# Performance work log

Measured on AMD Instinct MI355X. Metric: run time of the kernel, lower is better.

## Reference

```python
import jax, jax.numpy as jnp
import numpy as np

NEG = -1e30  # finite stand-in for -inf (keeps gradients NaN-free)
BLANK = 0    # PyTorch nn.CTCLoss default blank index


def setup_inputs() -> dict:
    key = jax.random.key(0)
    k1, k2, k3 = jax.random.split(key, 3)
    T, B, C, S = 512, 1024, 63, 25
    # model emits log-probabilities (log_softmax output), as nn.CTCLoss expects
    log_probs = jax.nn.log_softmax(jax.random.normal(k1, (T, B, C), jnp.float32), axis=-1)
    targets = jax.random.randint(k2, (B, S), 1, C, dtype=jnp.int32)        # labels in [1, C)
    target_lengths = jax.random.randint(k3, (B,), 10, S + 1, dtype=jnp.int32)
    return {"log_probs": log_probs, "targets": targets, "target_lengths": target_lengths}


def _ctc_loss(log_probs, targets, target_lengths):
    # log_probs: [T, B, C]; targets: [B, S] padded; target_lengths: [B]
    T, B, C = log_probs.shape
    S = targets.shape[1]
    L = 2 * S + 1  # extended target: blank-interleaved

    ext = jnp.zeros((B, L), targets.dtype).at[:, 1::2].set(targets)  # [B, L]
    prev2 = jnp.concatenate([jnp.full((B, 2), -1, ext.dtype), ext[:, :-2]], axis=1)
    skip = (ext != BLANK) & (ext != prev2)  # allow alpha[s-2] transition

    # t = 0 init: only positions 0 (blank) and 1 (first label) reachable
    lp0 = log_probs[0]  # [B, C]
    alpha0 = jnp.full((B, L), NEG, log_probs.dtype)
    alpha0 = alpha0.at[:, 0].set(lp0[:, BLANK])
    alpha0 = alpha0.at[:, 1].set(jnp.take_along_axis(lp0, ext[:, 1:2], axis=1)[:, 0])

    def step(alpha, lp_t):  # alpha: [B, L], lp_t: [B, C]
        lp_ext = jnp.take_along_axis(lp_t, ext, axis=1)  # [B, L]
        a1 = alpha
        a2 = jnp.pad(alpha[:, :-1], ((0, 0), (1, 0)), constant_values=NEG)
        a3 = jnp.where(skip, jnp.pad(alpha[:, :-2], ((0, 0), (2, 0)), constant_values=NEG), NEG)
        m = jnp.maximum(jnp.maximum(a1, a2), a3)
        new = m + jnp.log(jnp.exp(a1 - m) + jnp.exp(a2 - m) + jnp.exp(a3 - m)) + lp_ext
        return new, None

    alpha_T, _ = jax.lax.scan(step, alpha0, log_probs[1:])

    # log-likelihood = logaddexp of the last two reachable positions (2*len, 2*len-1)
    idx = jnp.stack([2 * target_lengths - 1, 2 * target_lengths], axis=1)  # [B, 2]
    a_fin = jnp.take_along_axis(alpha_T, idx, axis=1)
    ll = jnp.logaddexp(a_fin[:, 0], a_fin[:, 1])
    nll = -ll
    nll = jnp.where(nll > 0.5e30, 0.0, nll)  # zero_infinity=True
    # PyTorch reduction='mean': divide each loss by its target length, then batch mean
    return jnp.mean(nll / jnp.maximum(target_lengths, 1).astype(nll.dtype))


def reference(log_probs, targets, target_lengths):
    return _ctc_loss(log_probs, targets, target_lengths)
```

## Files before the change

### kernel.cpp

```cpp
#include <hip/hip_runtime.h>


#define TT 512
#define BB 1024
#define CC 63
#define SS 25
#define D  32
#define NEGV (-1e30f)
#define LN2F 0.69314718055994531f

__device__ __forceinline__ float shr1f(float x, float fill) {
  return __int_as_float(__builtin_amdgcn_update_dpp(
      __float_as_int(fill), __float_as_int(x), 0x138, 0xF, 0xF, false));
}
__device__ __forceinline__ int shr1i(int x, int fill) {
  return __builtin_amdgcn_update_dpp(fill, x, 0x138, 0xF, 0xF, false);
}
__device__ __forceinline__ float shl1f(float x, float fill) {
  return __int_as_float(__builtin_amdgcn_update_dpp(
      __float_as_int(fill), __float_as_int(x), 0x130, 0xF, 0xF, false));
}
__device__ __forceinline__ int shl1i(int x, int fill) {
  return __builtin_amdgcn_update_dpp(fill, x, 0x130, 0xF, 0xF, false);
}
__device__ __forceinline__ int iclamp126(int d) {
  return d < -126 ? -126 : (d > 126 ? 126 : d);
}

__global__ __launch_bounds__(256) void ctc_fb_kernel(
    const float* __restrict__ logp,
    const int* __restrict__ targets,
    const int* __restrict__ tlen,
    float* __restrict__ loss) {
  const int lane = threadIdx.x & 63;
  const int wid = threadIdx.x >> 6;
  const int pairIdx = wid >> 1;
  const int bwd = wid & 1;
  const int b = (blockIdx.x << 1) + pairIdx;
  const int* tg = targets + b * SS;
  const int len = tlen[b];

  int e = 0;
  float skf = 0.0f;
  float skf2 = 0.0f;
  if (lane & 1) {
    const int i = lane >> 1;
    if (i < SS) {
      e = tg[i];
      skf = (i == 0 || e != tg[i - 1]) ? 1.0f : 0.0f;
      if (i + 1 < SS) skf2 = (tg[i + 1] != tg[i]) ? 1.0f : 0.0f;
    }
  }

  const unsigned SB = (unsigned)(BB * CC) * 4u;
  const char* base = (const char*)logp;
  const unsigned off0 = (unsigned)(b * CC + e) * 4u;
#define LDF(O) (*(const float*)(base + (O)))

  __shared__ float la_s[2][64];

  float A, F1, F2m;
  int M2 = 0;
  float pf[D];
  unsigned offp;

  if (!bwd) {
    A = (lane <= 1) ? __expf(LDF(off0)) : 0.0f;
    F1 = 1.0f; F2m = skf;
    offp = off0 + SB;
#pragma unroll
    for (int j = 0; j < D; ++j) { pf[j] = LDF(offp); offp += SB; }

#define RENF() {                                               \
    int e2 = (int)(__float_as_uint(A) >> 23) - 127;            \
    A = ldexpf(A, -e2);                                        \
    int m2n = M2 + e2;                                         \
    int m2a = shr1i(m2n, 0);                                   \
    M2 = (A == 0.0f) ? m2a : m2n;                              \
    int s1 = shr1i(M2, 0), s2 = shr1i(s1, 0);                  \
    F1 = ldexpf(1.0f, iclamp126(s1 - M2));                     \
    F2m = skf * ldexpf(1.0f, iclamp126(s2 - M2));              \
  }
#define STEPF(J, PFLAG) {                                      \
    const float P = __expf(pf[(J)]);                           \
    const float c1 = P * F1, c2 = P * F2m;                     \
    const float a2 = shr1f(A, 0.0f);                           \
    const float pa = P * A;                                    \
    const float a3 = shr1f(a2, 0.0f);                          \
    A = fmaf(c2, a3, fmaf(c1, a2, pa));                        \
    if (PFLAG) { pf[(J)] = LDF(offp); offp += SB; }            \
    if (((J) & 15) == 15) RENF()                               \
  }

    for (int blk = 0; blk < 6; ++blk) {
#pragma unroll
      for (int j = 0; j < D; ++j) STEPF(j, true)
    }
#pragma unroll
    for (int j = 0; j < D; ++j) STEPF(j, j < 31)
#pragma unroll
    for (int j = 0; j < 31; ++j) STEPF(j, false)

    la_s[pairIdx][lane] = fmaxf((float)M2 * LN2F + logf(A), NEGV);
  } else {
    A = (lane == 2 * len - 1 || lane == 2 * len) ? 1.0f : 0.0f;
    F1 = 1.0f; F2m = skf2;
    offp = 511u * SB + off0;
#pragma unroll
    for (int j = 0; j < D; ++j) { pf[j] = LDF(offp); offp -= SB; }

#define RENB() {                                               \
    int e2 = (int)(__float_as_uint(A) >> 23) - 127;            \
    A = ldexpf(A, -e2);                                        \
    int m2n = M2 + e2;                                         \
    int m2a = shl1i(m2n, 0);                                   \
    M2 = (A == 0.0f) ? m2a : m2n;                              \
    int s1 = shl1i(M2, 0), s2 = shl1i(s1, 0);                  \
    F1 = ldexpf(1.0f, iclamp126(s1 - M2));                     \
    F2m = skf2 * ldexpf(1.0f, iclamp126(s2 - M2));             \
  }
#define STEPB(J, PFLAG) {                                      \
    const float P = __expf(pf[(J)]);                           \
    const float P1 = shl1f(P, 0.0f);                           \
    const float P2 = shl1f(P1, 0.0f);                          \
    const float c1 = F1 * P1, c2 = F2m * P2;                   \
    const float a1 = shl1f(A, 0.0f);                           \
    const float pa = P * A;                                    \
    const float a2 = shl1f(a1, 0.0f);                          \
    A = fmaf(c2, a2, fmaf(c1, a1, pa));                        \
    if (PFLAG) { pf[(J)] = LDF(offp); offp -= SB; }            \
    if (((J) & 15) == 15) RENB()                               \
  }

    for (int blk = 0; blk < 7; ++blk) {
#pragma unroll
      for (int j = 0; j < D; ++j) STEPB(j, true)
    }
#pragma unroll
    for (int j = 0; j < D; ++j) STEPB(j, false)
  }

  __syncthreads();

  if (bwd) {
    const float lb = fmaxf((float)M2 * LN2F + logf(A), NEGV);
    float v = (lane <= 50) ? la_s[pairIdx][lane] + lb : -2e30f;
    float m = v;
#pragma unroll
    for (int o = 32; o; o >>= 1) m = fmaxf(m, __shfl_xor(m, o));
    float s = __expf(v - m);
#pragma unroll
    for (int o = 32; o; o >>= 1) s += __shfl_xor(s, o);
    if (lane == 0) {
      const float ll = m + logf(s);
      float nll = -ll;
      if (!(nll <= 0.5e30f)) nll = 0.0f;
      const int dl = len > 1 ? len : 1;
      loss[b] = nll / (float)dl;
    }
  }
}

__global__ __launch_bounds__(256) void ctc_reduce_kernel(
    const float* __restrict__ loss, float* __restrict__ out) {
  float s = 0.f;
  for (int i = threadIdx.x; i < BB; i += 256) s += loss[i];
#pragma unroll
  for (int off = 32; off; off >>= 1) s += __shfl_down(s, off);
  __shared__ float sm[4];
  if ((threadIdx.x & 63) == 0) sm[threadIdx.x >> 6] = s;
  __syncthreads();
  if (threadIdx.x == 0) out[0] = (sm[0] + sm[1] + sm[2] + sm[3]) / (float)BB;
}

extern "C" void kernel_launch(void* const* d_in, const int* in_sizes, int n_in,
                              void* d_out, int out_size, void* d_ws, size_t ws_size,
                              hipStream_t stream) {
  const float* logp  = (const float*)d_in[0];
  const int* targets = (const int*)d_in[1];
  const int* tlen    = (const int*)d_in[2];
  float* out  = (float*)d_out;
  float* loss = (float*)d_ws;
  hipLaunchKernelGGL(ctc_fb_kernel, dim3(BB / 2), dim3(256), 0, stream,
                     logp, targets, tlen, loss);
  hipLaunchKernelGGL(ctc_reduce_kernel, dim3(1), dim3(256), 0, stream, loss, out);
}
```

Baseline: 32.92 us.

## Interleave forward and backward CTC recursions within a single wavefront per batch

Each wavefront now handles one batch element and runs both the forward alpha and backward beta recursions interleaved, instead of splitting them across two wavefronts joined through shared memory and a block barrier. The two independent dependency chains are meant to hide each other's DPP and FMA latency, and the barrier and LDS exchange go away. Prefetch depth per direction drops to 24 registers to fit both buffers. The cost is half as many wavefronts in total, so there is less latency hiding across waves, and register pressure goes up.

Result: faster. 31.96 us (median of 2 runs) (-2.9%).

```diff
diff --git a/kernel.cpp b/kernel.cpp
--- a/kernel.cpp
+++ b/kernel.cpp
@@ -5,7 +5,7 @@
 #define BB 1024
 #define CC 63
 #define SS 25
-#define D  32
+#define DP 24
 #define NEGV (-1e30f)
 #define LN2F 0.69314718055994531f
 
@@ -34,9 +34,7 @@
     float* __restrict__ loss) {
   const int lane = threadIdx.x & 63;
   const int wid = threadIdx.x >> 6;
-  const int pairIdx = wid >> 1;
-  const int bwd = wid & 1;
-  const int b = (blockIdx.x << 1) + pairIdx;
+  const int b = (blockIdx.x << 2) + wid;
   const int* tg = targets + b * SS;
   const int len = tlen[b];
 
@@ -55,109 +53,103 @@
   const unsigned SB = (unsigned)(BB * CC) * 4u;
   const char* base = (const char*)logp;
   const unsigned off0 = (unsigned)(b * CC + e) * 4u;
-#define LDF(O) (*(const float*)(base + (O)))
+#define LDR(O) (*(const float*)(base + (O)))
 
-  __shared__ float la_s[2][64];
+  float Af = (lane <= 1) ? __expf(LDR(off0)) : 0.0f;
+  int M2f = 0;
+  float F1f = 1.0f, F2f = skf;
+  float Ab = (lane == 2 * len - 1 || lane == 2 * len) ? 1.0f : 0.0f;
+  int M2b = 0;
+  float F1b = 1.0f, F2b = skf2;
 
-  float A, F1, F2m;
-  int M2 = 0;
-  float pf[D];
-  unsigned offp;
-
-  if (!bwd) {
-    A = (lane <= 1) ? __expf(LDF(off0)) : 0.0f;
-    F1 = 1.0f; F2m = skf;
-    offp = off0 + SB;
+  float pfF[DP], pfB[DP];
+  unsigned offF = off0 + SB;
+  unsigned offB = off0 + 511u * SB;
 #pragma unroll
-    for (int j = 0; j < D; ++j) { pf[j] = LDF(offp); offp += SB; }
+  for (int j = 0; j < DP; ++j) {
+    pfF[j] = LDR(offF); offF += SB;
+    pfB[j] = LDR(offB); offB -= SB;
+  }
 
 #define RENF() {                                               \
-    int e2 = (int)(__float_as_uint(A) >> 23) - 127;            \
-    A = ldexpf(A, -e2);                                        \
-    int m2n = M2 + e2;                                         \
+    int e2 = (int)(__float_as_uint(Af) >> 23) - 127;           \
+    Af = ldexpf(Af, -e2);                                      \
+    int m2n = M2f + e2;                                        \
     int m2a = shr1i(m2n, 0);                                   \
-    M2 = (A == 0.0f) ? m2a : m2n;                              \
-    int s1 = shr1i(M2, 0), s2 = shr1i(s1, 0);                  \
-    F1 = ldexpf(1.0f, iclamp126(s1 - M2));                     \
-    F2m = skf * ldexpf(1.0f, iclamp126(s2 - M2));              \
+    M2f = (Af == 0.0f) ? m2a : m2n;                            \
+    int s1 = shr1i(M2f, 0), s2 = shr1i(s1, 0);                 \
+    F1f = ldexpf(1.0f, iclamp126(s1 - M2f));                   \
+    F2f = skf * ldexpf(1.0f, iclamp126(s2 - M2f));             \
+  }
+#define RENB() {                                               \
+    int e2 = (int)(__float_as_uint(Ab) >> 23) - 127;           \
+    Ab = ldexpf(Ab, -e2);                                      \
+    int m2n = M2b + e2;                                        \
+    int m2a = shl1i(m2n, 0);                                   \
+    M2b = (Ab == 0.0f) ? m2a : m2n;                            \
+    int s1 = shl1i(M2b, 0), s2 = shl1i(s1, 0);                 \
+    F1b = ldexpf(1.0f, iclamp126(s1 - M2b));                   \
+    F2b = skf2 * ldexpf(1.0f, iclamp126(s2 - M2b));            \
   }
 #define STEPF(J, PFLAG) {                                      \
-    const float P = __expf(pf[(J)]);                           \
-    const float c1 = P * F1, c2 = P * F2m;                     \
-    const float a2 = shr1f(A, 0.0f);                           \
-    const float pa = P * A;                                    \
-    const float a3 = shr1f(a2, 0.0f);                          \
-    A = fmaf(c2, a3, fmaf(c1, a2, pa));                        \
-    if (PFLAG) { pf[(J)] = LDF(offp); offp += SB; }            \
-    if (((J) & 15) == 15) RENF()                               \
+    const float P = __expf(pfF[(J)]);                          \
+    const float c1 = P * F1f, c2 = P * F2f;                    \
+    const float x1 = shr1f(Af, 0.0f);                          \
+    const float pa = P * Af;                                   \
+    const float x2 = shr1f(x1, 0.0f);                          \
+    Af = fmaf(c2, x2, fmaf(c1, x1, pa));                       \
+    if (PFLAG) { pfF[(J)] = LDR(offF); offF += SB; }           \
+  }
+#define STEPB(J, PFLAG) {                                      \
+    const float P = __expf(pfB[(J)]);                          \
+    const float P1 = shl1f(P, 0.0f);                           \
+    const float P2 = shl1f(P1, 0.0f);                          \
+    const float c1 = F1b * P1, c2 = F2b * P2;                  \
+    const float y1 = shl1f(Ab, 0.0f);                          \
+    const float pb = P * Ab;                                   \
+    const float y2 = shl1f(y1, 0.0f);                          \
+    Ab = fmaf(c2, y2, fmaf(c1, y1, pb));                       \
+    if (PFLAG) { pfB[(J)] = LDR(offB); offB -= SB; }           \
   }
 
-    for (int blk = 0; blk < 6; ++blk) {
+  STEPB(0, true)
+
+  for (int blk = 0; blk < 9; ++blk) {
 #pragma unroll
-      for (int j = 0; j < D; ++j) STEPF(j, true)
+    for (int j = 0; j < DP; ++j) {
+      STEPF(j, true)
+      STEPB((j + 1) % DP, true)
+      if (j == 11 || j == 23) { RENF() RENB() }
     }
+  }
 #pragma unroll
-    for (int j = 0; j < D; ++j) STEPF(j, j < 31)
+  for (int j = 0; j < DP; ++j) {
+    STEPF(j, j <= 14)
+    STEPB((j + 1) % DP, j <= 14)
+    if (j == 11 || j == 23) { RENF() RENB() }
+  }
 #pragma unroll
-    for (int j = 0; j < 31; ++j) STEPF(j, false)
-
-    la_s[pairIdx][lane] = fmaxf((float)M2 * LN2F + logf(A), NEGV);
-  } else {
-    A = (lane == 2 * len - 1 || lane == 2 * len) ? 1.0f : 0.0f;
-    F1 = 1.0f; F2m = skf2;
-    offp = 511u * SB + off0;
-#pragma unroll
-    for (int j = 0; j < D; ++j) { pf[j] = LDF(offp); offp -= SB; }
-
-#define RENB() {                                               \
-    int e2 = (int)(__float_as_uint(A) >> 23) - 127;            \
-    A = ldexpf(A, -e2);                                        \
-    int m2n = M2 + e2;                                         \
-    int m2a = shl1i(m2n, 0);                                   \
-    M2 = (A == 0.0f) ? m2a : m2n;                              \
-    int s1 = shl1i(M2, 0), s2 = shl1i(s1, 0);                  \
-    F1 = ldexpf(1.0f, iclamp126(s1 - M2));                     \
-    F2m = skf2 * ldexpf(1.0f, iclamp126(s2 - M2));             \
-  }
-#define STEPB(J, PFLAG) {                                      \
-    const float P = __expf(pf[(J)]);                           \
-    const float P1 = shl1f(P, 0.0f);                           \
-    const float P2 = shl1f(P1, 0.0f);                          \
-    const float c1 = F1 * P1, c2 = F2m * P2;                   \
-    const float a1 = shl1f(A, 0.0f);                           \
-    const float pa = P * A;                                    \
-    const float a2 = shl1f(a1, 0.0f);                          \
-    A = fmaf(c2, a2, fmaf(c1, a1, pa));                        \
-    if (PFLAG) { pf[(J)] = LDF(offp); offp -= SB; }            \
-    if (((J) & 15) == 15) RENB()                               \
+  for (int j = 0; j < 15; ++j) {
+    STEPF(j, false)
+    STEPB(j + 1, false)
+    if (j == 11) { RENF() RENB() }
   }
 
-    for (int blk = 0; blk < 7; ++blk) {
+  const float laf = fmaxf((float)M2f * LN2F + logf(Af), NEGV);
+  const float lab = fmaxf((float)M2b * LN2F + logf(Ab), NEGV);
+  float v = (lane <= 50) ? laf + lab : -2e30f;
+  float m = v;
 #pragma unroll
-      for (int j = 0; j < D; ++j) STEPB(j, true)
-    }
+  for (int o = 32; o; o >>= 1) m = fmaxf(m, __shfl_xor(m, o));
+  float s = __expf(v - m);
 #pragma unroll
-    for (int j = 0; j < D; ++j) STEPB(j, false)
-  }
-
-  __syncthreads();
-
-  if (bwd) {
-    const float lb = fmaxf((float)M2 * LN2F + logf(A), NEGV);
-    float v = (lane <= 50) ? la_s[pairIdx][lane] + lb : -2e30f;
-    float m = v;
-#pragma unroll
-    for (int o = 32; o; o >>= 1) m = fmaxf(m, __shfl_xor(m, o));
-    float s = __expf(v - m);
-#pragma unroll
-    for (int o = 32; o; o >>= 1) s += __shfl_xor(s, o);
-    if (lane == 0) {
-      const float ll = m + logf(s);
-      float nll = -ll;
-      if (!(nll <= 0.5e30f)) nll = 0.0f;
-      const int dl = len > 1 ? len : 1;
-      loss[b] = nll / (float)dl;
-    }
+  for (int o = 32; o; o >>= 1) s += __shfl_xor(s, o);
+  if (lane == 0) {
+    const float ll = m + logf(s);
+    float nll = -ll;
+    if (!(nll <= 0.5e30f)) nll = 0.0f;
+    const int dl = len > 1 ? len : 1;
+    loss[b] = nll / (float)dl;
   }
 }
 
@@ -181,7 +173,7 @@
   const int* tlen    = (const int*)d_in[2];
   float* out  = (float*)d_out;
   float* loss = (float*)d_ws;
-  hipLaunchKernelGGL(ctc_fb_kernel, dim3(BB / 2), dim3(256), 0, stream,
+  hipLaunchKernelGGL(ctc_fb_kernel, dim3(BB / 4), dim3(256), 0, stream,
                      logp, targets, tlen, loss);
   hipLaunchKernelGGL(ctc_reduce_kernel, dim3(1), dim3(256), 0, stream, loss, out);
 }
```
